# Optimization experiments

Hardware: AMD Instinct MI355X
Metric: run time of the kernel (lower is better)

## Reference

```python
import jax, jax.numpy as jnp
import numpy as np

V, E, H2, K = 50000, 64, 128, 3
H = H2 // 2  # per-direction LSTM hidden
B, T = 256, 512


def setup_inputs() -> dict:
    key = jax.random.key(0)
    ks = jax.random.split(key, 12)
    s = 0.1
    return {
        "x": jax.random.randint(ks[0], (B, T), 0, V, dtype=jnp.int32),
        "y": jax.random.randint(ks[1], (B, T), 0, K, dtype=jnp.int32),
        "mask": jnp.ones((B, T), dtype=bool),
        "emb": jax.random.normal(ks[2], (V, E), jnp.float32) * s,
        "w_ih_f": jax.random.normal(ks[3], (4 * H, E), jnp.float32) * s,
        "w_hh_f": jax.random.normal(ks[4], (4 * H, H), jnp.float32) * s,
        "b_ih_f": jnp.zeros((4 * H,), jnp.float32),
        "b_hh_f": jnp.zeros((4 * H,), jnp.float32),
        "w_ih_b": jax.random.normal(ks[5], (4 * H, E), jnp.float32) * s,
        "w_hh_b": jax.random.normal(ks[6], (4 * H, H), jnp.float32) * s,
        "b_ih_b": jnp.zeros((4 * H,), jnp.float32),
        "b_hh_b": jnp.zeros((4 * H,), jnp.float32),
        "fc_w": jax.random.normal(ks[7], (K, H2), jnp.float32) * s,
        "fc_b": jnp.zeros((K,), jnp.float32),
        "start_t": jax.random.normal(ks[8], (K,), jnp.float32) * s,
        "end_t": jax.random.normal(ks[9], (K,), jnp.float32) * s,
        "trans": jax.random.normal(ks[10], (K, K), jnp.float32) * s,
    }


def _lstm(x_tbe, w_ih, w_hh, b_ih, b_hh):
    # x_tbe: [T,B,E] -> hidden states [T,B,H]; torch gate order i,f,g,o
    pre = jnp.einsum('tbe,ge->tbg', x_tbe, w_ih) + b_ih + b_hh  # [T,B,4H]
    Bb = x_tbe.shape[1]
    Hh = w_hh.shape[1]

    def step(carry, p):
        h, c = carry
        g = p + h @ w_hh.T
        i, f, gg, o = jnp.split(g, 4, axis=-1)
        c = jax.nn.sigmoid(f) * c + jax.nn.sigmoid(i) * jnp.tanh(gg)
        h = jax.nn.sigmoid(o) * jnp.tanh(c)
        return (h, c), h

    init = (jnp.zeros((Bb, Hh), pre.dtype), jnp.zeros((Bb, Hh), pre.dtype))
    _, hs = jax.lax.scan(step, init, pre)
    return hs


def _emissions(x, emb, w_ih_f, w_hh_f, b_ih_f, b_hh_f,
               w_ih_b, w_hh_b, b_ih_b, b_hh_b, fc_w, fc_b):
    h = emb[x]                      # [B,T,E]
    h = jnp.swapaxes(h, 0, 1)       # [T,B,E] (time-major)
    hf = _lstm(h, w_ih_f, w_hh_f, b_ih_f, b_hh_f)            # [T,B,H]
    hb = _lstm(h[::-1], w_ih_b, w_hh_b, b_ih_b, b_hh_b)[::-1]  # [T,B,H]
    out = jnp.concatenate([hf, hb], axis=-1)                 # [T,B,2H]
    return jnp.einsum('tbh,kh->tbk', out, fc_w) + fc_b       # [T,B,K]


def _crf_nll(em, y, mask, start_t, end_t, trans):
    # em: [T,B,K]; y, mask: [B,T]. Returns -mean log-likelihood (torchcrf, reduction='mean').
    y_t = y.T                      # [T,B]
    m = mask.T.astype(em.dtype)    # [T,B]
    Bb = y_t.shape[1]
    bar = jnp.arange(Bb)
    # numerator (gold path score)
    score = start_t[y_t[0]] + em[0, bar, y_t[0]]
    trans_sc = trans[y_t[:-1], y_t[1:]]                                 # [T-1,B]
    em_sc = jnp.take_along_axis(em, y_t[..., None], axis=-1)[..., 0]    # [T,B]
    score = score + jnp.sum(m[1:] * (trans_sc + em_sc[1:]), axis=0)
    seq_ends = mask.T.astype(jnp.int32).sum(axis=0) - 1                 # [B]
    last_tags = y_t[seq_ends, bar]
    numerator = score + end_t[last_tags]
    # log-partition via forward algorithm (scan over time, K=3 states)
    alpha0 = start_t[None, :] + em[0]   # [B,K]

    def step(alpha, inp):
        em_i, m_i = inp
        nxt = jax.nn.logsumexp(alpha[:, :, None] + trans[None] + em_i[:, None, :], axis=1)
        return jnp.where(m_i[:, None] > 0, nxt, alpha), None

    alpha, _ = jax.lax.scan(step, alpha0, (em[1:], m[1:]))
    logZ = jax.nn.logsumexp(alpha + end_t[None, :], axis=1)   # [B]
    llh = numerator - logZ
    return -jnp.mean(llh)


def reference(x, y, mask, emb, w_ih_f, w_hh_f, b_ih_f, b_hh_f,
              w_ih_b, w_hh_b, b_ih_b, b_hh_b, fc_w, fc_b,
              start_t, end_t, trans):
    em = _emissions(x, emb, w_ih_f, w_hh_f, b_ih_f, b_hh_f,
                    w_ih_b, w_hh_b, b_ih_b, b_hh_b, fc_w, fc_b)
    return _crf_nll(em, y, mask, start_t, end_t, trans)
```

## Files before the change

### kernel.cpp

```cpp
#include <hip/hip_runtime.h>
#include <hip/hip_fp16.h>

static constexpr int TT = 512;
static constexpr int BB = 256;
static constexpr int EE = 64;
static constexpr int HH = 64;
static constexpr int KK = 3;

typedef _Float16 hv2   __attribute__((ext_vector_type(2)));
typedef _Float16 half8 __attribute__((ext_vector_type(8)));
typedef float    f32x4 __attribute__((ext_vector_type(4)));
typedef int      i32x4 __attribute__((ext_vector_type(4)));

__device__ __forceinline__ hv2 bch2(int u) { return __builtin_bit_cast(hv2, u); }
__device__ __forceinline__ hv2 rlh2(int v, int l) {
  return __builtin_bit_cast(hv2, __builtin_amdgcn_readlane(v, l));
}
__device__ __forceinline__ unsigned pk(float a, float b) {
  return __builtin_bit_cast(unsigned, __builtin_amdgcn_cvt_pkrtz(a, b));
}
__device__ __forceinline__ float lse3(float x0, float x1, float x2) {
  float m = fmaxf(fmaxf(x0, x1), x2);
  return m + __logf(__expf(x0 - m) + __expf(x1 - m) + __expf(x2 - m));
}
__device__ __forceinline__ void lds_barrier() {
  __asm__ volatile("s_waitcnt lgkmcnt(0)\n\ts_barrier" ::: "memory");
}

#define MFMA16(A, B, C) __builtin_amdgcn_mfma_f32_16x16x32_f16(A, B, C, 0, 0, 0)

#define LWF(dstv, row, src, kslice) { \
    const float* base = (src) + (size_t)(row) * 64 + 32 * (kslice) + quad * 8; \
    float4 u = *(const float4*)base; float4 v = *(const float4*)(base + 4); \
    i32x4 iv = {(int)pk(u.x, u.y), (int)pk(u.z, u.w), \
                (int)pk(v.x, v.y), (int)pk(v.z, v.w)}; \
    dstv = __builtin_bit_cast(half8, iv); }

#define TRSEL(ypv, ycv) ((ypv) == 0 ? ((ycv) == 0 ? t00 : (ycv) == 1 ? t01 : t02) \
                       : (ypv) == 1 ? ((ycv) == 0 ? t10 : (ycv) == 1 ? t11 : t12) \
                       :              ((ycv) == 0 ? t20 : (ycv) == 1 ? t21 : t22))


__global__ __launch_bounds__(256, 1) void pre_kernel(
    const int* __restrict__ x, const float* __restrict__ emb,
    const float* __restrict__ w_ih_f, const float* __restrict__ b_ih_f,
    const float* __restrict__ b_hh_f,
    const float* __restrict__ w_ih_b, const float* __restrict__ b_ih_b,
    const float* __restrict__ b_hh_b,
    unsigned* __restrict__ pre) {
  const int tid  = threadIdx.x;
  const int wv   = tid >> 6;
  const int l    = tid & 63;
  const int quad = l >> 4;
  const int c    = l & 15;
  const int tg   = blockIdx.x & 31;
  const int bg   = (blockIdx.x >> 5) & 63;
  const int dir  = blockIdx.x >> 11;
  const int b0   = bg * 4;
  const int t0   = tg * 16;

  const float* wih = dir ? w_ih_b : w_ih_f;
  const float* bih = dir ? b_ih_b : b_ih_f;
  const float* bhh = dir ? b_hh_b : b_hh_f;

  const int gd = 16 * wv + c;
  half8 W00, W01, W10, W11, W20, W21, W30, W31;
  LWF(W00, gd,       wih, 0) LWF(W01, gd,       wih, 1)
  LWF(W10, gd + 64,  wih, 0) LWF(W11, gd + 64,  wih, 1)
  LWF(W20, gd + 128, wih, 0) LWF(W21, gd + 128, wih, 1)
  LWF(W30, gd + 192, wih, 0) LWF(W31, gd + 192, wih, 1)
  const float bias0 = bih[gd]       + bhh[gd];
  const float bias1 = bih[gd + 64]  + bhh[gd + 64];
  const float bias2 = bih[gd + 128] + bhh[gd + 128];
  const float bias3 = bih[gd + 192] + bhh[gd + 192];

  __shared__ __align__(16) _Float16 xs[4][16][72];
  { const int q4 = tid & 3, bi = (tid >> 2) & 3, sg = tid >> 4;
    const int t2 = t0 + sg;
    const int ts = dir ? (TT - 1 - t2) : t2;
    const int row = x[(b0 + bi) * TT + ts];
    const float4* er = (const float4*)(emb + (size_t)row * EE + q4 * 16);
    float4 u0 = er[0], u1 = er[1], u2 = er[2], u3 = er[3];
    i32x4 va = {(int)pk(u0.x, u0.y), (int)pk(u0.z, u0.w),
                (int)pk(u1.x, u1.y), (int)pk(u1.z, u1.w)};
    i32x4 vb = {(int)pk(u2.x, u2.y), (int)pk(u2.z, u2.w),
                (int)pk(u3.x, u3.y), (int)pk(u3.z, u3.w)};
    _Float16* xr = &xs[sg >> 2][(sg & 3) * 4 + bi][q4 * 16];
    *(i32x4*)xr       = va;
    *(i32x4*)(xr + 8) = vb;
  }
  __syncthreads();

  unsigned* pb = pre + (size_t)(dir * 64 + bg) * 512 * 512;
#pragma unroll
  for (int g = 0; g < 4; ++g) {
    const half8 xa0 = *(const half8*)&xs[g][c][quad * 8];
    const half8 xa1 = *(const half8*)&xs[g][c][32 + quad * 8];
    f32x4 a0 = {bias0, bias0, bias0, bias0};
    f32x4 a1 = {bias1, bias1, bias1, bias1};
    f32x4 a2 = {bias2, bias2, bias2, bias2};
    f32x4 a3 = {bias3, bias3, bias3, bias3};
    a0 = MFMA16(xa0, W00, a0); a0 = MFMA16(xa1, W01, a0);
    a1 = MFMA16(xa0, W10, a1); a1 = MFMA16(xa1, W11, a1);
    a2 = MFMA16(xa0, W20, a2); a2 = MFMA16(xa1, W21, a2);
    a3 = MFMA16(xa0, W30, a3); a3 = MFMA16(xa1, W31, a3);
    unsigned* ps = pb + (size_t)(t0 + g * 4 + quad) * 512 + wv * 128 + c * 2;
#pragma unroll
    for (int r = 0; r < 4; ++r) {
      uint2 o; o.x = pk(a0[r], a1[r]); o.y = pk(a2[r], a3[r]);
      *(uint2*)(ps + r * 32) = o;
    }
  }
}

__global__ __launch_bounds__(256, 1) void lstm_rec(
    const unsigned* __restrict__ pre,
    const float* __restrict__ w_hh_f, const float* __restrict__ w_hh_b,
    __half* __restrict__ h16) {
  const int tid  = threadIdx.x;
  const int wv   = tid >> 6;
  const int l    = tid & 63;
  const int quad = l >> 4;
  const int c    = l & 15;
  const int bg   = blockIdx.x & 63;
  const int dir  = blockIdx.x >> 6;
  const int b0   = bg * 4;
  const int dirb4 = dir * BB + b0;

  const float* whh = dir ? w_hh_b : w_hh_f;

  __shared__ __align__(16) _Float16 hbuf[2][16][72];

  const int gd = 16 * wv + c;
  half8 W00, W01, W10, W11, W20, W21, W30, W31;
  LWF(W00, gd,       whh, 0) LWF(W01, gd,       whh, 1)
  LWF(W10, gd + 64,  whh, 0) LWF(W11, gd + 64,  whh, 1)
  LWF(W20, gd + 128, whh, 0) LWF(W21, gd + 128, whh, 1)
  LWF(W30, gd + 192, whh, 0) LWF(W31, gd + 192, whh, 1)

  for (int i = tid; i < 2 * 16 * 72 / 2; i += 256) ((unsigned*)hbuf)[i] = 0u;

  const unsigned* preb = pre + (size_t)(dir * 64 + bg) * 512 * 512;
  const int loff = wv * 128 + l * 2;
  uint2 P0 = *(const uint2*)(preb + 0 * 512 + loff);
  uint2 P1 = *(const uint2*)(preb + 1 * 512 + loff);
  uint2 P2 = *(const uint2*)(preb + 2 * 512 + loff);
  uint2 P3 = *(const uint2*)(preb + 3 * 512 + loff);
  const uint2* q0 = (const uint2*)(preb + 4 * 512 + loff);
  const uint2* q1 = (const uint2*)(preb + 5 * 512 + loff);
  const uint2* q2 = (const uint2*)(preb + 6 * 512 + loff);
  const uint2* q3 = (const uint2*)(preb + 7 * 512 + loff);

  const bool hvalid = (c & 3) == 0;
  const int  hbi    = c >> 2;
  const int  u_first = (wv == 0) ? 4 : wv;
  const int  tsp0 = dir ? (TT - u_first) : (u_first - 1);
  __half* hptr = h16 + ((size_t)(dirb4 + hbi) * TT + tsp0) * 64;
  const int hstep = dir ? -256 : 256;

  __syncthreads();

  float cs = 0.f;
  f32x4 a0 = {0.f, 0.f, 0.f, 0.f};
  f32x4 a1 = a0, a2 = a0, a3 = a0;

#define STEPB(st, BK) { \
    const int nb = ((st) + 1) & 1; \
    { hv2 p0 = bch2((int)P##BK.x), p1 = bch2((int)P##BK.y); \
      a0[0] = (float)p0.x; a1[0] = (float)p0.y; \
      a2[0] = (float)p1.x; a3[0] = (float)p1.y; } \
    P##BK = *q##BK; q##BK += 1024;    \
    const half8 ha0 = *(const half8*)&hbuf[(st) & 1][c][quad * 8]; \
    const half8 ha1 = *(const half8*)&hbuf[(st) & 1][c][32 + quad * 8]; \
    if (wv == ((st) & 3) && hvalid && (((st) != 0) || ci)) { \
      *(half8*)(hptr + quad * 8)      = ha0; \
      *(half8*)(hptr + 32 + quad * 8) = ha1; \
      hptr += hstep; } \
    a0 = MFMA16(ha0, W00, a0); a1 = MFMA16(ha0, W10, a1); \
    a2 = MFMA16(ha0, W20, a2); a3 = MFMA16(ha0, W30, a3); \
    a0 = MFMA16(ha1, W01, a0); a1 = MFMA16(ha1, W11, a1); \
    a2 = MFMA16(ha1, W21, a2); a3 = MFMA16(ha1, W31, a3); \
    { float iv = a0[0], fv = a1[0], gv = a2[0], ov = a3[0]; \
      float ef = __expf(-fv); \
      float sf = __builtin_amdgcn_rcpf(1.f + ef); \
      float ei = __expf(-iv); \
      float eg = __expf(-2.f * gv); \
      float itg = (1.f - eg) * __builtin_amdgcn_rcpf((1.f + ei) * (1.f + eg)); \
      float cn = sf * cs + itg; \
      float eo = __expf(-ov); \
      float ec = __expf(-2.f * cn); \
      float hn = (1.f - ec) * __builtin_amdgcn_rcpf((1.f + eo) * (1.f + ec)); \
      cs = cn; \
      hbuf[nb][quad * 4][gd] = (_Float16)hn; } \
    lds_barrier(); }

  for (int ci = 0; ci < 64; ++ci) {
    STEPB(0, 0) STEPB(1, 1) STEPB(2, 2) STEPB(3, 3)
    STEPB(4, 0) STEPB(5, 1) STEPB(6, 2) STEPB(7, 3)
  }

  if (wv == 3 && hvalid) {
    const half8 hf0 = *(const half8*)&hbuf[0][c][quad * 8];
    const half8 hf1 = *(const half8*)&hbuf[0][c][32 + quad * 8];
    int tsl = dir ? 0 : (TT - 1);
    __half* dst = h16 + ((size_t)(dirb4 + hbi) * TT + tsl) * 64;
    *(half8*)(dst + quad * 8)      = hf0;
    *(half8*)(dst + 32 + quad * 8) = hf1;
  }
}

__global__ void emis_kernel(
    const __half* __restrict__ h16, const float* __restrict__ fc_w,
    const float* __restrict__ fc_b, float4* __restrict__ em4) {
  const int b   = blockIdx.x & 255;
  const int th  = blockIdx.x >> 8;
  const int tid = threadIdx.x;
  const int l   = tid & 63;

  int T0, T1, T2;
  { float2 v0 = *(const float2*)&fc_w[0 * 128 + 2 * l];
    float2 v1 = *(const float2*)&fc_w[1 * 128 + 2 * l];
    float2 v2 = *(const float2*)&fc_w[2 * 128 + 2 * l];
    T0 = (int)pk(v0.x, v0.y); T1 = (int)pk(v1.x, v1.y); T2 = (int)pk(v2.x, v2.y); }
  const float fb0 = fc_b[0], fb1 = fc_b[1], fb2 = fc_b[2];

  const int t = th * 256 + tid;
  const uint4* hf = (const uint4*)(h16 + ((size_t)b * TT + t) * 64);
  const uint4* hb = (const uint4*)(h16 + ((size_t)(BB + b) * TT + t) * 64);
  float a0 = fb0, a1 = fb1, a2 = fb2;
#define EMDOT(v, jbase) { \
    a0 = __builtin_amdgcn_fdot2(bch2((int)(v)), rlh2(T0, (jbase)), a0, false); \
    a1 = __builtin_amdgcn_fdot2(bch2((int)(v)), rlh2(T1, (jbase)), a1, false); \
    a2 = __builtin_amdgcn_fdot2(bch2((int)(v)), rlh2(T2, (jbase)), a2, false); }
#pragma unroll
  for (int cidx = 0; cidx < 8; ++cidx) {
    uint4 v = hf[cidx];
    EMDOT(v.x, cidx * 4 + 0) EMDOT(v.y, cidx * 4 + 1)
    EMDOT(v.z, cidx * 4 + 2) EMDOT(v.w, cidx * 4 + 3)
  }
#pragma unroll
  for (int cidx = 0; cidx < 8; ++cidx) {
    uint4 v = hb[cidx];
    EMDOT(v.x, 32 + cidx * 4 + 0) EMDOT(v.y, 32 + cidx * 4 + 1)
    EMDOT(v.z, 32 + cidx * 4 + 2) EMDOT(v.w, 32 + cidx * 4 + 3)
  }
  float4 o; o.x = a0; o.y = a1; o.z = a2; o.w = 0.f;
  em4[(size_t)t * BB + b] = o;
}

__global__ __launch_bounds__(256, 1) void crf_chunks(
    const int* __restrict__ y, const float4* __restrict__ em4,
    const float* __restrict__ trans, float4* __restrict__ cw4) {
  const int c = blockIdx.x;
  const int b = threadIdx.x;
  __shared__ float tr[9];
  if (threadIdx.x < 9) tr[threadIdx.x] = trans[threadIdx.x];
  __syncthreads();
  const float t00 = tr[0], t01 = tr[1], t02 = tr[2];
  const float t10 = tr[3], t11 = tr[4], t12 = tr[5];
  const float t20 = tr[6], t21 = tr[7], t22 = tr[8];

  const int t0 = (c == 0) ? 1 : c * 8;
  const int te = c * 8 + 8;
  const int* yb = y + (size_t)b * TT;

  float4 e = em4[(size_t)t0 * BB + b];
  float m00 = t00 + e.x, m01 = t01 + e.y, m02 = t02 + e.z;
  float m10 = t10 + e.x, m11 = t11 + e.y, m12 = t12 + e.z;
  float m20 = t20 + e.x, m21 = t21 + e.y, m22 = t22 + e.z;
  int yp = yb[t0 - 1];
  int yc = yb[t0];
  float sc = TRSEL(yp, yc) + (yc == 0 ? e.x : yc == 1 ? e.y : e.z);
  yp = yc;

  for (int t = t0 + 1; t < te; ++t) {
    float4 et = em4[(size_t)t * BB + b];
    float n00 = et.x + lse3(m00 + t00, m01 + t10, m02 + t20);
    float n01 = et.y + lse3(m00 + t01, m01 + t11, m02 + t21);
    float n02 = et.z + lse3(m00 + t02, m01 + t12, m02 + t22);
    float n10 = et.x + lse3(m10 + t00, m11 + t10, m12 + t20);
    float n11 = et.y + lse3(m10 + t01, m11 + t11, m12 + t21);
    float n12 = et.z + lse3(m10 + t02, m11 + t12, m12 + t22);
    float n20 = et.x + lse3(m20 + t00, m21 + t10, m22 + t20);
    float n21 = et.y + lse3(m20 + t01, m21 + t11, m22 + t21);
    float n22 = et.z + lse3(m20 + t02, m21 + t12, m22 + t22);
    m00 = n00; m01 = n01; m02 = n02;
    m10 = n10; m11 = n11; m12 = n12;
    m20 = n20; m21 = n21; m22 = n22;
    yc = yb[t];
    sc += TRSEL(yp, yc) + (yc == 0 ? et.x : yc == 1 ? et.y : et.z);
    yp = yc;
  }

  float4 o0 = {m00, m01, m02, m10};
  float4 o1 = {m11, m12, m20, m21};
  float4 o2 = {m22, sc, 0.f, 0.f};
  cw4[(size_t)(c * 3 + 0) * BB + b] = o0;
  cw4[(size_t)(c * 3 + 1) * BB + b] = o1;
  cw4[(size_t)(c * 3 + 2) * BB + b] = o2;
}

__global__ __launch_bounds__(64, 1) void crf_combine(
    const int* __restrict__ y, const float4* __restrict__ em4,
    const float4* __restrict__ cw4,
    const float* __restrict__ start_t, const float* __restrict__ end_t,
    float* __restrict__ out) {
  const int tid = threadIdx.x;
  const int b   = blockIdx.x * 64 + tid;

  const float s0 = start_t[0], s1 = start_t[1], s2 = start_t[2];
  const float en0 = end_t[0], en1 = end_t[1], en2 = end_t[2];
  const int* yb = y + (size_t)b * TT;

  float4 e0 = em4[b];
  const int y0 = yb[0], yl = yb[TT - 1];
  float a0 = s0 + e0.x, a1 = s1 + e0.y, a2 = s2 + e0.z;
  float score = (y0 == 0 ? s0 : y0 == 1 ? s1 : s2) +
                (y0 == 0 ? e0.x : y0 == 1 ? e0.y : e0.z) +
                (yl == 0 ? en0 : yl == 1 ? en1 : en2);

  float4 A0 = cw4[b], A1 = cw4[BB + b], A2 = cw4[2 * BB + b];
  for (int c = 0; c < 64; ++c) {
    float4 B0 = A0, B1 = A1, B2 = A2;
    if (c < 63) {
      const size_t base = (size_t)((c + 1) * 3) * BB + b;
      B0 = cw4[base]; B1 = cw4[base + BB]; B2 = cw4[base + 2 * BB];
    }
    score += A2.y;
    float na0 = lse3(a0 + A0.x, a1 + A0.w, a2 + A1.z);
    float na1 = lse3(a0 + A0.y, a1 + A1.x, a2 + A1.w);
    float na2 = lse3(a0 + A0.z, a1 + A1.y, a2 + A2.x);
    a0 = na0; a1 = na1; a2 = na2;
    A0 = B0; A1 = B1; A2 = B2;
  }

  const float logZ = lse3(a0 + en0, a1 + en1, a2 + en2);
  float llh = score - logZ;
#pragma unroll
  for (int m = 32; m >= 1; m >>= 1) llh += __shfl_xor(llh, m, 64);
  if (tid == 0) atomicAdd(out, -llh * (1.0f / 256.0f));
}

extern "C" void kernel_launch(void* const* d_in, const int* in_sizes, int n_in,
                              void* d_out, int out_size, void* d_ws, size_t ws_size,
                              hipStream_t stream) {
  const int*   x      = (const int*)d_in[0];
  const int*   y      = (const int*)d_in[1];
  const float* emb    = (const float*)d_in[3];
  const float* w_ih_f = (const float*)d_in[4];
  const float* w_hh_f = (const float*)d_in[5];
  const float* b_ih_f = (const float*)d_in[6];
  const float* b_hh_f = (const float*)d_in[7];
  const float* w_ih_b = (const float*)d_in[8];
  const float* w_hh_b = (const float*)d_in[9];
  const float* b_ih_b = (const float*)d_in[10];
  const float* b_hh_b = (const float*)d_in[11];
  const float* fc_w   = (const float*)d_in[12];
  const float* fc_b   = (const float*)d_in[13];
  const float* start_t= (const float*)d_in[14];
  const float* end_t  = (const float*)d_in[15];
  const float* trans  = (const float*)d_in[16];

  float* out = (float*)d_out;
  hipMemsetAsync(d_out, 0, sizeof(float), stream);

  const size_t pre_bytes = (size_t)128 * 512 * 512 * 4;
  const size_t h16_bytes = (size_t)2 * BB * TT * 64 * 2;
  unsigned* pre = (unsigned*)d_ws;
  __half*   h16 = (__half*)((char*)d_ws + pre_bytes);
  float4*   em4 = (float4*)((char*)d_ws + pre_bytes + h16_bytes);
  float4*   cw4 = (float4*)d_ws;

  pre_kernel<<<4096, 256, 0, stream>>>(x, emb, w_ih_f, b_ih_f, b_hh_f,
                                       w_ih_b, b_ih_b, b_hh_b, pre);
  lstm_rec<<<128, 256, 0, stream>>>(pre, w_hh_f, w_hh_b, h16);
  emis_kernel<<<512, 256, 0, stream>>>(h16, fc_w, fc_b, em4);
  crf_chunks<<<64, 256, 0, stream>>>(y, em4, trans, cw4);
  crf_combine<<<4, 64, 0, stream>>>(y, em4, cw4, start_t, end_t, out);
}
```

Baseline: 331.3 us.

## Fuse input projection into LSTM recurrence with producer waves feeding an LDS ring

```diff
diff --git a/kernel.cpp b/kernel.cpp
--- a/kernel.cpp
+++ b/kernel.cpp
@@ -40,81 +40,12 @@
                        : (ypv) == 1 ? ((ycv) == 0 ? t10 : (ycv) == 1 ? t11 : t12) \
                        :              ((ycv) == 0 ? t20 : (ycv) == 1 ? t21 : t22))
 
-
-__global__ __launch_bounds__(256, 1) void pre_kernel(
+__global__ __launch_bounds__(512, 1) void lstm_fused(
     const int* __restrict__ x, const float* __restrict__ emb,
     const float* __restrict__ w_ih_f, const float* __restrict__ b_ih_f,
     const float* __restrict__ b_hh_f,
     const float* __restrict__ w_ih_b, const float* __restrict__ b_ih_b,
     const float* __restrict__ b_hh_b,
-    unsigned* __restrict__ pre) {
-  const int tid  = threadIdx.x;
-  const int wv   = tid >> 6;
-  const int l    = tid & 63;
-  const int quad = l >> 4;
-  const int c    = l & 15;
-  const int tg   = blockIdx.x & 31;
-  const int bg   = (blockIdx.x >> 5) & 63;
-  const int dir  = blockIdx.x >> 11;
-  const int b0   = bg * 4;
-  const int t0   = tg * 16;
-
-  const float* wih = dir ? w_ih_b : w_ih_f;
-  const float* bih = dir ? b_ih_b : b_ih_f;
-  const float* bhh = dir ? b_hh_b : b_hh_f;
-
-  const int gd = 16 * wv + c;
-  half8 W00, W01, W10, W11, W20, W21, W30, W31;
-  LWF(W00, gd,       wih, 0) LWF(W01, gd,       wih, 1)
-  LWF(W10, gd + 64,  wih, 0) LWF(W11, gd + 64,  wih, 1)
-  LWF(W20, gd + 128, wih, 0) LWF(W21, gd + 128, wih, 1)
-  LWF(W30, gd + 192, wih, 0) LWF(W31, gd + 192, wih, 1)
-  const float bias0 = bih[gd]       + bhh[gd];
-  const float bias1 = bih[gd + 64]  + bhh[gd + 64];
-  const float bias2 = bih[gd + 128] + bhh[gd + 128];
-  const float bias3 = bih[gd + 192] + bhh[gd + 192];
-
-  __shared__ __align__(16) _Float16 xs[4][16][72];
-  { const int q4 = tid & 3, bi = (tid >> 2) & 3, sg = tid >> 4;
-    const int t2 = t0 + sg;
-    const int ts = dir ? (TT - 1 - t2) : t2;
-    const int row = x[(b0 + bi) * TT + ts];
-    const float4* er = (const float4*)(emb + (size_t)row * EE + q4 * 16);
-    float4 u0 = er[0], u1 = er[1], u2 = er[2], u3 = er[3];
-    i32x4 va = {(int)pk(u0.x, u0.y), (int)pk(u0.z, u0.w),
-                (int)pk(u1.x, u1.y), (int)pk(u1.z, u1.w)};
-    i32x4 vb = {(int)pk(u2.x, u2.y), (int)pk(u2.z, u2.w),
-                (int)pk(u3.x, u3.y), (int)pk(u3.z, u3.w)};
-    _Float16* xr = &xs[sg >> 2][(sg & 3) * 4 + bi][q4 * 16];
-    *(i32x4*)xr       = va;
-    *(i32x4*)(xr + 8) = vb;
-  }
-  __syncthreads();
-
-  unsigned* pb = pre + (size_t)(dir * 64 + bg) * 512 * 512;
-#pragma unroll
-  for (int g = 0; g < 4; ++g) {
-    const half8 xa0 = *(const half8*)&xs[g][c][quad * 8];
-    const half8 xa1 = *(const half8*)&xs[g][c][32 + quad * 8];
-    f32x4 a0 = {bias0, bias0, bias0, bias0};
-    f32x4 a1 = {bias1, bias1, bias1, bias1};
-    f32x4 a2 = {bias2, bias2, bias2, bias2};
-    f32x4 a3 = {bias3, bias3, bias3, bias3};
-    a0 = MFMA16(xa0, W00, a0); a0 = MFMA16(xa1, W01, a0);
-    a1 = MFMA16(xa0, W10, a1); a1 = MFMA16(xa1, W11, a1);
-    a2 = MFMA16(xa0, W20, a2); a2 = MFMA16(xa1, W21, a2);
-    a3 = MFMA16(xa0, W30, a3); a3 = MFMA16(xa1, W31, a3);
-    unsigned* ps = pb + (size_t)(t0 + g * 4 + quad) * 512 + wv * 128 + c * 2;
-#pragma unroll
-    for (int r = 0; r < 4; ++r) {
-      uint2 o; o.x = pk(a0[r], a1[r]); o.y = pk(a2[r], a3[r]);
-      *(uint2*)(ps + r * 32) = o;
-    }
-  }
-}
-
-__global__ __launch_bounds__(256, 1) void lstm_rec(
-    const unsigned* __restrict__ pre,
     const float* __restrict__ w_hh_f, const float* __restrict__ w_hh_b,
     __half* __restrict__ h16) {
   const int tid  = threadIdx.x;
@@ -128,28 +59,70 @@
   const int dirb4 = dir * BB + b0;
 
   const float* whh = dir ? w_hh_b : w_hh_f;
+  const float* wih = dir ? w_ih_b : w_ih_f;
+  const float* bih = dir ? b_ih_b : b_ih_f;
+  const float* bhh = dir ? b_hh_b : b_hh_f;
 
   __shared__ __align__(16) _Float16 hbuf[2][16][72];
-
-  const int gd = 16 * wv + c;
-  half8 W00, W01, W10, W11, W20, W21, W30, W31;
-  LWF(W00, gd,       whh, 0) LWF(W01, gd,       whh, 1)
-  LWF(W10, gd + 64,  whh, 0) LWF(W11, gd + 64,  whh, 1)
-  LWF(W20, gd + 128, whh, 0) LWF(W21, gd + 128, whh, 1)
-  LWF(W30, gd + 192, whh, 0) LWF(W31, gd + 192, whh, 1)
-
-  for (int i = tid; i < 2 * 16 * 72 / 2; i += 256) ((unsigned*)hbuf)[i] = 0u;
-
-  const unsigned* preb = pre + (size_t)(dir * 64 + bg) * 512 * 512;
-  const int loff = wv * 128 + l * 2;
-  uint2 P0 = *(const uint2*)(preb + 0 * 512 + loff);
-  uint2 P1 = *(const uint2*)(preb + 1 * 512 + loff);
-  uint2 P2 = *(const uint2*)(preb + 2 * 512 + loff);
-  uint2 P3 = *(const uint2*)(preb + 3 * 512 + loff);
-  const uint2* q0 = (const uint2*)(preb + 4 * 512 + loff);
-  const uint2* q1 = (const uint2*)(preb + 5 * 512 + loff);
-  const uint2* q2 = (const uint2*)(preb + 6 * 512 + loff);
-  const uint2* q3 = (const uint2*)(preb + 7 * 512 + loff);
+  __shared__ __align__(16) unsigned preLDS[16 * 512];
+
+  const int rowbase = 16 * (wv & 3) + c;
+  const float* wsrc = (wv < 4) ? whh : wih;
+  half8 B0, B1, B2, B3, B4, B5, B6, B7;
+  LWF(B0, rowbase,       wsrc, 0) LWF(B1, rowbase,       wsrc, 1)
+  LWF(B2, rowbase + 64,  wsrc, 0) LWF(B3, rowbase + 64,  wsrc, 1)
+  LWF(B4, rowbase + 128, wsrc, 0) LWF(B5, rowbase + 128, wsrc, 1)
+  LWF(B6, rowbase + 192, wsrc, 0) LWF(B7, rowbase + 192, wsrc, 1)
+  const float bias0 = bih[rowbase]       + bhh[rowbase];
+  const float bias1 = bih[rowbase + 64]  + bhh[rowbase + 64];
+  const float bias2 = bih[rowbase + 128] + bhh[rowbase + 128];
+  const float bias3 = bih[rowbase + 192] + bhh[rowbase + 192];
+
+  for (int i = tid; i < 2 * 16 * 72 / 2; i += 512) ((unsigned*)hbuf)[i] = 0u;
+
+  int xr0 = 0, xr1 = 0;
+  float4 E0, E1, E2, E3, E4, E5, E6, E7;
+  const int* xpb = x + (b0 + (c & 3)) * TT;
+
+#define XLOAD(g) { \
+    int t2a = (g) * 8 + (c >> 2);     if (t2a > 511) t2a = 511; \
+    int t2b = (g) * 8 + 4 + (c >> 2); if (t2b > 511) t2b = 511; \
+    xr0 = xpb[dir ? (511 - t2a) : t2a]; \
+    xr1 = xpb[dir ? (511 - t2b) : t2b]; }
+
+#define EMBISSUE() { \
+    const float* ea = emb + ((size_t)xr0 << 6) + quad * 8; \
+    E0 = *(const float4*)ea;        E1 = *(const float4*)(ea + 4); \
+    E2 = *(const float4*)(ea + 32); E3 = *(const float4*)(ea + 36); \
+    const float* eb = emb + ((size_t)xr1 << 6) + quad * 8; \
+    E4 = *(const float4*)eb;        E5 = *(const float4*)(eb + 4); \
+    E6 = *(const float4*)(eb + 32); E7 = *(const float4*)(eb + 36); }
+
+#define PPASS(g, p, EA, EB, EC, ED) { \
+    i32x4 v0 = {(int)pk(EA.x, EA.y), (int)pk(EA.z, EA.w), \
+                (int)pk(EB.x, EB.y), (int)pk(EB.z, EB.w)}; \
+    i32x4 v1 = {(int)pk(EC.x, EC.y), (int)pk(EC.z, EC.w), \
+                (int)pk(ED.x, ED.y), (int)pk(ED.z, ED.w)}; \
+    half8 xa0 = __builtin_bit_cast(half8, v0); \
+    half8 xa1 = __builtin_bit_cast(half8, v1); \
+    f32x4 p0 = {bias0, bias0, bias0, bias0}; \
+    f32x4 p1 = {bias1, bias1, bias1, bias1}; \
+    f32x4 p2 = {bias2, bias2, bias2, bias2}; \
+    f32x4 p3 = {bias3, bias3, bias3, bias3}; \
+    p0 = MFMA16(xa0, B0, p0); p0 = MFMA16(xa1, B1, p0); \
+    p1 = MFMA16(xa0, B2, p1); p1 = MFMA16(xa1, B3, p1); \
+    p2 = MFMA16(xa0, B4, p2); p2 = MFMA16(xa1, B5, p2); \
+    p3 = MFMA16(xa0, B6, p3); p3 = MFMA16(xa1, B7, p3); \
+    const int s_ = (g) * 8 + (p) * 4 + quad; \
+    char* wp = (char*)preLDS + (s_ & 15) * 2048 + (wv & 3) * 512 + c * 8; \
+    { uint2 o; o.x = pk(p0[0], p1[0]); o.y = pk(p2[0], p3[0]); \
+      *(uint2*)(wp + 0 * 128) = o; } \
+    { uint2 o; o.x = pk(p0[1], p1[1]); o.y = pk(p2[1], p3[1]); \
+      *(uint2*)(wp + 1 * 128) = o; } \
+    { uint2 o; o.x = pk(p0[2], p1[2]); o.y = pk(p2[2], p3[2]); \
+      *(uint2*)(wp + 2 * 128) = o; } \
+    { uint2 o; o.x = pk(p0[3], p1[3]); o.y = pk(p2[3], p3[3]); \
+      *(uint2*)(wp + 3 * 128) = o; } }
 
   const bool hvalid = (c & 3) == 0;
   const int  hbi    = c >> 2;
@@ -157,29 +130,52 @@
   const int  tsp0 = dir ? (TT - u_first) : (u_first - 1);
   __half* hptr = h16 + ((size_t)(dirb4 + hbi) * TT + tsp0) * 64;
   const int hstep = dir ? -256 : 256;
-
+  const int gd = 16 * wv + c;
+
+  const char* plc = (const char*)preLDS;
+  const int loff8 = (wv & 3) * 512 + l * 8;
+  int off0 = 4 * 2048 + loff8, off1 = 5 * 2048 + loff8;
+  int off2 = 6 * 2048 + loff8, off3 = 7 * 2048 + loff8;
+
+  if (wv >= 4) {
+    XLOAD(0) EMBISSUE()
+    PPASS(0, 0, E0, E1, E2, E3) PPASS(0, 1, E4, E5, E6, E7)
+    XLOAD(1) EMBISSUE()
+    PPASS(1, 0, E0, E1, E2, E3) PPASS(1, 1, E4, E5, E6, E7)
+    XLOAD(2) EMBISSUE()
+    XLOAD(3)
+  }
   __syncthreads();
+
+  uint2 P0 = {0, 0}, P1 = P0, P2 = P0, P3 = P0;
+  if (wv < 4) {
+    P0 = *(const uint2*)(plc + 0 * 2048 + loff8);
+    P1 = *(const uint2*)(plc + 1 * 2048 + loff8);
+    P2 = *(const uint2*)(plc + 2 * 2048 + loff8);
+    P3 = *(const uint2*)(plc + 3 * 2048 + loff8);
+  }
 
   float cs = 0.f;
   f32x4 a0 = {0.f, 0.f, 0.f, 0.f};
   f32x4 a1 = a0, a2 = a0, a3 = a0;
 
-#define STEPB(st, BK) { \
+#define CSTEP(st, BK) { \
     const int nb = ((st) + 1) & 1; \
     { hv2 p0 = bch2((int)P##BK.x), p1 = bch2((int)P##BK.y); \
       a0[0] = (float)p0.x; a1[0] = (float)p0.y; \
       a2[0] = (float)p1.x; a3[0] = (float)p1.y; } \
-    P##BK = *q##BK; q##BK += 1024;    \
+    P##BK = *(const uint2*)(plc + off##BK); \
+    off##BK = (off##BK + 8192) & 32767; \
     const half8 ha0 = *(const half8*)&hbuf[(st) & 1][c][quad * 8]; \
     const half8 ha1 = *(const half8*)&hbuf[(st) & 1][c][32 + quad * 8]; \
     if (wv == ((st) & 3) && hvalid && (((st) != 0) || ci)) { \
       *(half8*)(hptr + quad * 8)      = ha0; \
       *(half8*)(hptr + 32 + quad * 8) = ha1; \
       hptr += hstep; } \
-    a0 = MFMA16(ha0, W00, a0); a1 = MFMA16(ha0, W10, a1); \
-    a2 = MFMA16(ha0, W20, a2); a3 = MFMA16(ha0, W30, a3); \
-    a0 = MFMA16(ha1, W01, a0); a1 = MFMA16(ha1, W11, a1); \
-    a2 = MFMA16(ha1, W21, a2); a3 = MFMA16(ha1, W31, a3); \
+    a0 = MFMA16(ha0, B0, a0); a1 = MFMA16(ha0, B2, a1); \
+    a2 = MFMA16(ha0, B4, a2); a3 = MFMA16(ha0, B6, a3); \
+    a0 = MFMA16(ha1, B1, a0); a1 = MFMA16(ha1, B3, a1); \
+    a2 = MFMA16(ha1, B5, a2); a3 = MFMA16(ha1, B7, a3); \
     { float iv = a0[0], fv = a1[0], gv = a2[0], ov = a3[0]; \
       float ef = __expf(-fv); \
       float sf = __builtin_amdgcn_rcpf(1.f + ef); \
@@ -191,12 +187,25 @@
       float ec = __expf(-2.f * cn); \
       float hn = (1.f - ec) * __builtin_amdgcn_rcpf((1.f + eo) * (1.f + ec)); \
       cs = cn; \
-      hbuf[nb][quad * 4][gd] = (_Float16)hn; } \
-    lds_barrier(); }
+      hbuf[nb][quad * 4][gd] = (_Float16)hn; } }
 
   for (int ci = 0; ci < 64; ++ci) {
-    STEPB(0, 0) STEPB(1, 1) STEPB(2, 2) STEPB(3, 3)
-    STEPB(4, 0) STEPB(5, 1) STEPB(6, 2) STEPB(7, 3)
+    if (wv < 4) CSTEP(0, 0)
+    lds_barrier();
+    if (wv < 4) CSTEP(1, 1) else PPASS(ci + 2, 0, E0, E1, E2, E3)
+    lds_barrier();
+    if (wv < 4) CSTEP(2, 2)
+    lds_barrier();
+    if (wv < 4) CSTEP(3, 3)
+    lds_barrier();
+    if (wv < 4) CSTEP(4, 0) else PPASS(ci + 2, 1, E4, E5, E6, E7)
+    lds_barrier();
+    if (wv < 4) CSTEP(5, 1) else EMBISSUE()
+    lds_barrier();
+    if (wv < 4) CSTEP(6, 2) else XLOAD(ci + 4)
+    lds_barrier();
+    if (wv < 4) CSTEP(7, 3)
+    lds_barrier();
   }
 
   if (wv == 3 && hvalid) {
@@ -364,16 +373,15 @@
   float* out = (float*)d_out;
   hipMemsetAsync(d_out, 0, sizeof(float), stream);
 
-  const size_t pre_bytes = (size_t)128 * 512 * 512 * 4;
   const size_t h16_bytes = (size_t)2 * BB * TT * 64 * 2;
-  unsigned* pre = (unsigned*)d_ws;
-  __half*   h16 = (__half*)((char*)d_ws + pre_bytes);
-  float4*   em4 = (float4*)((char*)d_ws + pre_bytes + h16_bytes);
-  float4*   cw4 = (float4*)d_ws;
-
-  pre_kernel<<<4096, 256, 0, stream>>>(x, emb, w_ih_f, b_ih_f, b_hh_f,
-                                       w_ih_b, b_ih_b, b_hh_b, pre);
-  lstm_rec<<<128, 256, 0, stream>>>(pre, w_hh_f, w_hh_b, h16);
+  const size_t em4_bytes = (size_t)TT * BB * 16;
+  __half* h16 = (__half*)d_ws;
+  float4* em4 = (float4*)((char*)d_ws + h16_bytes);
+  float4* cw4 = (float4*)((char*)d_ws + h16_bytes + em4_bytes);
+
+  lstm_fused<<<128, 512, 0, stream>>>(x, emb, w_ih_f, b_ih_f, b_hh_f,
+                                      w_ih_b, b_ih_b, b_hh_b,
+                                      w_hh_f, w_hh_b, h16);
   emis_kernel<<<512, 256, 0, stream>>>(h16, fc_w, fc_b, em4);
   crf_chunks<<<64, 256, 0, stream>>>(y, em4, trans, cw4);
   crf_combine<<<4, 64, 0, stream>>>(y, em4, cw4, start_t, end_t, out);
```

Measured after the change: 290.1 us. -12.4%, faster.
